# Optimization experiments

Measured on AMD Instinct MI355X. Metric: run time of the kernel, lower is better.

The kernel has to match this reference:

```python
import jax, jax.numpy as jnp
import numpy as np
import math

HIDDEN = 2048
NUM_HEADS = 16
NUM_KV_HEADS = 4
HEAD_DIM = 128
GROUPS = NUM_HEADS // NUM_KV_HEADS
BATCH = 1
SEQ = 4096
THETA = 10000.0


def _rope(x):
    # x: [B, h, S, D], interleaved-pair rotation as in the torch module
    seq = x.shape[2]
    freqs = 1.0 / (THETA ** (jnp.arange(0, HEAD_DIM, 2, dtype=jnp.float32) / HEAD_DIM))  # [D/2]
    angles = jnp.arange(seq, dtype=jnp.float32)[:, None] * freqs[None, :]  # [S, D/2]
    cos = jnp.cos(angles)[None, None]  # [1,1,S,D/2]
    sin = jnp.sin(angles)[None, None]
    x1 = x[..., 0::2]
    x2 = x[..., 1::2]
    # stack along new last axis then flatten -> interleaved layout
    rot = jnp.stack([x1 * cos - x2 * sin, x1 * sin + x2 * cos], axis=-1)
    return rot.reshape(x.shape)


def setup_inputs() -> dict:
    key = jax.random.key(0)
    kx, kq, kk, kv, ko = jax.random.split(key, 5)
    scale = 0.02
    x = jax.random.normal(kx, (BATCH, SEQ, HIDDEN), dtype=jnp.float32)
    Wq = jax.random.normal(kq, (NUM_HEADS * HEAD_DIM, HIDDEN), dtype=jnp.float32) * scale
    Wk = jax.random.normal(kk, (NUM_KV_HEADS * HEAD_DIM, HIDDEN), dtype=jnp.float32) * scale
    Wv = jax.random.normal(kv, (NUM_KV_HEADS * HEAD_DIM, HIDDEN), dtype=jnp.float32) * scale
    Wo = jax.random.normal(ko, (HIDDEN, NUM_HEADS * HEAD_DIM), dtype=jnp.float32) * scale
    return {"x": x, "Wq": Wq, "Wk": Wk, "Wv": Wv, "Wo": Wo}


def reference(x, Wq, Wk, Wv, Wo):
    B, S, _ = x.shape
    q = (x @ Wq.T).reshape(B, S, NUM_HEADS, HEAD_DIM).transpose(0, 2, 1, 3)      # [B,16,S,D]
    k = (x @ Wk.T).reshape(B, S, NUM_KV_HEADS, HEAD_DIM).transpose(0, 2, 1, 3)   # [B,4,S,D]
    v = (x @ Wv.T).reshape(B, S, NUM_KV_HEADS, HEAD_DIM).transpose(0, 2, 1, 3)
    q = _rope(q)
    k = _rope(k)
    # GQA: repeat_interleave KV heads across the group dim
    k = jnp.repeat(k, GROUPS, axis=1)  # [B,16,S,D]
    v = jnp.repeat(v, GROUPS, axis=1)
    scale = 1.0 / math.sqrt(HEAD_DIM)
    scores = jnp.einsum("bhqd,bhkd->bhqk", q, k) * scale  # [B,16,S,S]
    causal = jnp.triu(jnp.ones((S, S), dtype=bool), k=1)
    scores = jnp.where(causal[None, None], jnp.float32(-jnp.inf), scores)
    attn = jax.nn.softmax(scores, axis=-1)
    out = jnp.einsum("bhqk,bhkd->bhqd", attn, v)           # [B,16,S,D]
    out = out.transpose(0, 2, 1, 3).reshape(B, S, NUM_HEADS * HEAD_DIM)
    return out @ Wo.T
```

## Files before the change

### kernel.cpp

```cpp
#include <hip/hip_runtime.h>
#include <hip/hip_bf16.h>

typedef unsigned short u16;
typedef unsigned int u32;
typedef short short8 __attribute__((ext_vector_type(8)));
typedef unsigned short ushort4v __attribute__((ext_vector_type(4)));
typedef float f32x4 __attribute__((ext_vector_type(4)));
typedef float f32x16 __attribute__((ext_vector_type(16)));
typedef u32 u32x4 __attribute__((ext_vector_type(4)));

#define SEQN 4096
#define HID 2048
#define NH 16
#define NKV 4
#define HD 128
#define QDIM 2048
#define KVD 512
#define QKVS 3072

static __device__ __forceinline__ float bf2f(u16 u){
  unsigned x = ((unsigned)u) << 16; float f; __builtin_memcpy(&f, &x, 4); return f;
}
static __device__ __forceinline__ u16 f2bf(float f){
  unsigned x; __builtin_memcpy(&x, &f, 4);
  x += 0x7fffu + ((x >> 16) & 1u);
  return (u16)(x >> 16);
}
static __device__ __forceinline__ u32 pk2(float a, float b){
  return (u32)f2bf(a) | ((u32)f2bf(b) << 16);
}

__global__ __launch_bounds__(256) void cvt_kernel(const float* __restrict__ in, u16* __restrict__ out, int n4){
  int i = blockIdx.x * 256 + threadIdx.x;
  if (i >= n4) return;
  f32x4 v = ((const f32x4*)in)[i];
  ushort4v o;
  o.x = f2bf(v.x); o.y = f2bf(v.y); o.z = f2bf(v.z); o.w = f2bf(v.w);
  ((ushort4v*)out)[i] = o;
}

__global__ __launch_bounds__(256) void rope_kernel(u16* __restrict__ X, int stride, int nheads, int total){
  int idx = blockIdx.x * 256 + threadIdx.x;
  if (idx >= total) return;
  int i = idx & 63;
  int rest = idx >> 6;
  int h = rest % nheads;
  int s = rest / nheads;
  float freq = expf(-0.14391156831212788f * (float)i);
  float ang = (float)s * freq;
  float c = cosf(ang), sn = sinf(ang);
  u16* p = X + (size_t)s * stride + (size_t)h * HD + 2 * i;
  float x1 = bf2f(p[0]), x2 = bf2f(p[1]);
  p[0] = f2bf(x1 * c - x2 * sn);
  p[1] = f2bf(x1 * sn + x2 * c);
}

__global__ __launch_bounds__(256) void vtrans_kernel(const u16* __restrict__ V, int vstride, u16* __restrict__ VTg){
  __shared__ u16 T[64][72];
  const int s0 = blockIdx.x * 64;
  const int c0 = blockIdx.y * 64;
  const int tid = threadIdx.x;
  const int sl = tid & 63, ch = tid >> 6;
  const u16* src = V + (size_t)(s0 + sl) * vstride + c0 + ch * 16;
  *(short8*)&T[sl][ch * 16]     = *(const short8*)(src);
  *(short8*)&T[sl][ch * 16 + 8] = *(const short8*)(src + 8);
  __syncthreads();
#pragma unroll
  for (int it = 0; it < 16; it++){
    int c = it * 4 + ch;
    VTg[(size_t)(c0 + c) * SEQN + s0 + sl] = T[sl][c];
  }
}

static __device__ __forceinline__ void gload16(const void* g, void* l){
  __builtin_amdgcn_global_load_lds((const __attribute__((address_space(1))) void*)g,
                                   (__attribute__((address_space(3))) void*)l, 16, 0, 0);
}

template<int F32OUT>
__global__ __launch_bounds__(256) void gemm_kernel(const u16* __restrict__ A, const u16* __restrict__ B,
                                                   void* __restrict__ Cout, int M, int N, int Kd, int ldc){
  __shared__ alignas(16) u16 As[128 * 32];
  __shared__ alignas(16) u16 Bs[128 * 32];
  const int tid = threadIdx.x;
  const int w = tid >> 6, l = tid & 63;
  const int wr = w >> 1, wc = w & 1;
  const int lc = l & 15, lg = l >> 4;
  const int tm = blockIdx.x * 128, tn = blockIdx.y * 128;

  const int srow = w * 32 + (l >> 2);
  const int scol = (l & 3) * 8;
  const u16* Ag = A + (size_t)(tm + srow) * Kd + scol;
  const u16* Bg = B + (size_t)(tn + srow) * Kd + scol;
  u16* As0 = As + (w * 2) * 512;
  u16* Bs0 = Bs + (w * 2) * 512;

  f32x4 acc[4][4] = {};

  for (int k0 = 0; k0 < Kd; k0 += 32){
    gload16(Ag + k0,                    As0);
    gload16(Ag + k0 + (size_t)16 * Kd,  As0 + 512);
    gload16(Bg + k0,                    Bs0);
    gload16(Bg + k0 + (size_t)16 * Kd,  Bs0 + 512);
    __syncthreads();
    short8 a[4], b[4];
#pragma unroll
    for (int mi = 0; mi < 4; mi++) a[mi] = *(const short8*)&As[(wr*64 + mi*16 + lc) * 32 + lg*8];
#pragma unroll
    for (int ni = 0; ni < 4; ni++) b[ni] = *(const short8*)&Bs[(wc*64 + ni*16 + lc) * 32 + lg*8];
#pragma unroll
    for (int mi = 0; mi < 4; mi++)
#pragma unroll
      for (int ni = 0; ni < 4; ni++)
        acc[mi][ni] = __builtin_amdgcn_mfma_f32_16x16x32_bf16(a[mi], b[ni], acc[mi][ni], 0, 0, 0);
    __syncthreads();
  }

#pragma unroll
  for (int mi = 0; mi < 4; mi++)
#pragma unroll
    for (int ni = 0; ni < 4; ni++)
#pragma unroll
      for (int r = 0; r < 4; r++){
        int row = tm + wr*64 + mi*16 + lg*4 + r;
        int col = tn + wc*64 + ni*16 + lc;
        float v = acc[mi][ni][r];
        if (F32OUT) ((float*)Cout)[(size_t)row * ldc + col] = v;
        else        ((u16*)Cout)[(size_t)row * ldc + col] = f2bf(v);
      }
}

__global__ __launch_bounds__(256, 2) void attn_kernel(const u16* __restrict__ Qg, const u16* __restrict__ Kgb,
                                                      const u16* __restrict__ VTg, u16* __restrict__ Aout,
                                                      u16* __restrict__ PO, float* __restrict__ mP,
                                                      float* __restrict__ LP){
  __shared__ alignas(16) char pool[65536];

  const int pr  = blockIdx.x;
  const int h   = blockIdx.y;
  const int s   = blockIdx.z;
  const int kvh = h >> 2;
  const int tid = threadIdx.x;
  const int w = tid >> 6, l = tid & 63;
  const int q5 = l & 31;
  const int hi = l >> 5;
  const int hi4 = hi * 4;
  const float csc = 0.12751743f;

  const u16* Ksrc[4];
  const u16* Vsrc[4];
#pragma unroll
  for (int i = 0; i < 4; i++){
    int blk = w * 4 + i;
    int row = blk * 4 + (l >> 4);
    int cg  = (l & 15) ^ (row & 15);
    Ksrc[i] = Kgb + (size_t)row * QKVS + kvh * HD + cg * 8;
    int d   = blk * 8 + (l >> 3);
    int cv  = (l & 7) ^ (d & 7);
    Vsrc[i] = VTg + (size_t)(kvh * 128 + d) * SEQN + cv * 8;
  }

  auto issueTile = [&](int b, int kv0){
    char* Ksb = pool + b * 32768;
    char* VTb = Ksb + 16384;
#pragma unroll
    for (int i = 0; i < 4; i++)
      gload16(Ksrc[i] + (size_t)kv0 * QKVS, Ksb + (w * 4 + i) * 1024);
#pragma unroll
    for (int i = 0; i < 4; i++)
      gload16(Vsrc[i] + kv0, VTb + (w * 4 + i) * 1024);
  };

  const int qlo = pr, qhi = 31 - pr;
  int nseg, sq[2], st0[2], st1[2], smode[2];
  if (s == 0){
    nseg = 2;
    sq[0] = qlo; st0[0] = 0;           st1[0] = 2 * pr + 2;   smode[0] = 0;
    sq[1] = qhi; st0[1] = 0;           st1[1] = 31 - 2 * pr;  smode[1] = 1;
  } else {
    nseg = 1;
    sq[0] = qhi; st0[0] = 31 - 2 * pr; st1[0] = 64 - 2 * pr;  smode[0] = 2;
  }

  for (int sg = 0; sg < nseg; sg++){
    const int qt = sq[sg], t0 = st0[sg], t1 = st1[sg], mode = smode[sg];
    const int qbase = qt * 128 + w * 32;
    const int qa    = qbase + q5;

    short8 qf[8];
    {
      const u16* qp = Qg + (size_t)(qbase + q5) * QKVS + h * HD + hi * 8;
#pragma unroll
      for (int k0 = 0; k0 < 8; k0++) qf[k0] = *(const short8*)(qp + k0 * 16);
    }

    f32x16 Ov[4] = {};
    float Lrow = 0.f;
    float ms = -1e30f;

    auto computeTile = [&](int b, int kv0){
      if (kv0 > qbase + 31) return;
      char* Ksb = pool + b * 32768;
      char* VTb = Ksb + 16384;
      f32x16 Sv[2] = {};
#pragma unroll
      for (int k0 = 0; k0 < 8; k0++){
#pragma unroll
        for (int nb = 0; nb < 2; nb++){
          int kvr = nb * 32 + q5;
          short8 kf = *(const short8*)(Ksb + kvr * 256 + (((k0 * 2 + hi) ^ (kvr & 15)) << 4));
          Sv[nb] = __builtin_amdgcn_mfma_f32_32x32x16_bf16(kf, qf[k0], Sv[nb], 0, 0, 0);
        }
      }
      if (kv0 + 63 > qbase){
#pragma unroll
        for (int nb = 0; nb < 2; nb++)
#pragma unroll
          for (int r = 0; r < 16; r++){
            int kva = kv0 + nb * 32 + (r & 3) + 8 * (r >> 2) + hi4;
            if (kva > qa) Sv[nb][r] = -1e30f;
          }
      }
      float tm = -3e38f;
#pragma unroll
      for (int nb = 0; nb < 2; nb++)
#pragma unroll
        for (int r = 0; r < 16; r++) tm = fmaxf(tm, Sv[nb][r]);
      tm = fmaxf(tm, __shfl_xor(tm, 32));
      float tms = tm * csc;
      if (!__all(tms - ms <= 8.f)){
        float nms = fmaxf(ms, tms);
        float al = __builtin_amdgcn_exp2f(ms - nms);
        ms = nms;
        Lrow *= al;
#pragma unroll
        for (int nb = 0; nb < 4; nb++)
#pragma unroll
          for (int r = 0; r < 16; r++) Ov[nb][r] *= al;
      }
      float ts = 0.f;
#pragma unroll
      for (int nb = 0; nb < 2; nb++)
#pragma unroll
        for (int r = 0; r < 16; r++){
          float p = __builtin_amdgcn_exp2f(__builtin_fmaf(Sv[nb][r], csc, -ms));
          Sv[nb][r] = p;
          ts += p;
        }
      ts += __shfl_xor(ts, 32);
      Lrow += ts;
#pragma unroll
      for (int kc = 0; kc < 4; kc++){
        const int nb = kc >> 1, rb = (kc & 1) * 8;
        u32 Aw = pk2(Sv[nb][rb + 0], Sv[nb][rb + 1]);
        u32 Bw = pk2(Sv[nb][rb + 2], Sv[nb][rb + 3]);
        u32 Cw = pk2(Sv[nb][rb + 4], Sv[nb][rb + 5]);
        u32 Dw = pk2(Sv[nb][rb + 6], Sv[nb][rb + 7]);
        u32 sAw = __shfl_xor(Aw, 32);
        u32 sBw = __shfl_xor(Bw, 32);
        u32 sCw = __shfl_xor(Cw, 32);
        u32 sDw = __shfl_xor(Dw, 32);
        u32 w0 = hi ? sCw : Aw;
        u32 w1 = hi ? sDw : Bw;
        u32 w2 = hi ? Cw : sAw;
        u32 w3 = hi ? Dw : sBw;
        u32x4 pw4 = {w0, w1, w2, w3};
        short8 pf = *(short8*)&pw4;
#pragma unroll
        for (int nbd = 0; nbd < 4; nbd++){
          int drow = nbd * 32 + q5;
          short8 vf = *(const short8*)(VTb + drow * 128 + (((kc * 2 + hi) ^ (drow & 7)) << 4));
          Ov[nbd] = __builtin_amdgcn_mfma_f32_32x32x16_bf16(vf, pf, Ov[nbd], 0, 0, 0);
        }
      }
    };

    __syncthreads();
    issueTile(0, t0 * 64);
    __syncthreads();
    int cur = 0;
    for (int t = t0; t < t1; t++){
      if (t + 1 < t1) issueTile(cur ^ 1, (t + 1) * 64);
      computeTile(cur, t * 64);
      __syncthreads();
      cur ^= 1;
    }

    u16* Ew = (u16*)(pool + w * 8704);
    float rl = (mode == 0) ? (1.f / Lrow) : 1.f;
#pragma unroll
    for (int nbd = 0; nbd < 4; nbd++)
#pragma unroll
      for (int r = 0; r < 16; r += 2){
        int d = nbd * 32 + (r & 3) + 8 * (r >> 2) + hi4;
        u32 wpk = pk2(Ov[nbd][r] * rl, Ov[nbd][r + 1] * rl);
        *(u32*)((char*)Ew + q5 * 272 + d * 2) = wpk;
      }
    if (mode == 0){
#pragma unroll
      for (int pass = 0; pass < 8; pass++){
        int q2 = pass * 4 + (l >> 4);
        short8 ov = *(const short8*)((char*)Ew + q2 * 272 + (l & 15) * 16);
        *(short8*)(Aout + (size_t)(qbase + q2) * QDIM + h * HD + (l & 15) * 8) = ov;
      }
    } else {
      const int p = mode - 1;
      u16* dstb = PO + ((size_t)((p * 16 + pr) * NH + h) * 128) * 128;
#pragma unroll
      for (int pass = 0; pass < 8; pass++){
        int q2 = pass * 4 + (l >> 4);
        short8 ov = *(const short8*)((char*)Ew + q2 * 272 + (l & 15) * 16);
        *(short8*)(dstb + (size_t)(w * 32 + q2) * 128 + (l & 15) * 8) = ov;
      }
      if (hi == 0){
        int idx = ((p * 16 + pr) * NH + h) * 128 + w * 32 + q5;
        mP[idx] = ms;
        LP[idx] = Lrow;
      }
    }
  }
}

__global__ __launch_bounds__(256) void combine_kernel(const u16* __restrict__ PO, const float* __restrict__ mP,
                                                      const float* __restrict__ LP, u16* __restrict__ Aout){
  const int pr = blockIdx.x;
  const int h  = blockIdx.y;
  const int tid = threadIdx.x;
  const int r  = tid >> 1;
  const int dh = (tid & 1) * 64;
  const int qhi = 31 - pr;
  const int idx0 = ((0 * 16 + pr) * NH + h) * 128 + r;
  const int idx1 = ((1 * 16 + pr) * NH + h) * 128 + r;
  float m0 = mP[idx0], m1 = mP[idx1];
  float L0 = LP[idx0], L1 = LP[idx1];
  float M = fmaxf(m0, m1);
  float a0 = __builtin_amdgcn_exp2f(m0 - M);
  float a1 = __builtin_amdgcn_exp2f(m1 - M);
  float rl = 1.f / (L0 * a0 + L1 * a1);
  const u16* o0 = PO + (size_t)idx0 * 128 + dh;
  const u16* o1 = PO + (size_t)idx1 * 128 + dh;
  u16* dst = Aout + (size_t)(qhi * 128 + r) * QDIM + h * HD + dh;
#pragma unroll
  for (int ch = 0; ch < 8; ch++){
    short8 v0 = *(const short8*)(o0 + ch * 8);
    short8 v1 = *(const short8*)(o1 + ch * 8);
    short8 ov;
#pragma unroll
    for (int j = 0; j < 8; j++)
      ov[j] = (short)f2bf((bf2f((u16)v0[j]) * a0 + bf2f((u16)v1[j]) * a1) * rl);
    *(short8*)(dst + ch * 8) = ov;
  }
}

extern "C" void kernel_launch(void* const* d_in, const int* in_sizes, int n_in,
                              void* d_out, int out_size, void* d_ws, size_t ws_size,
                              hipStream_t stream){
  const float* x  = (const float*)d_in[0];
  const float* Wq = (const float*)d_in[1];
  const float* Wk = (const float*)d_in[2];
  const float* Wv = (const float*)d_in[3];
  const float* Wo = (const float*)d_in[4];

  char* p = (char*)d_ws;
  u16* xb    = (u16*)p; p += (size_t)SEQN * HID * 2;
  u16* Wqkvb = (u16*)p; p += (size_t)QKVS * HID * 2;
  u16* Wob   = (u16*)p; p += (size_t)HID * QDIM * 2;
  u16* QKVb  = (u16*)p; p += (size_t)SEQN * QKVS * 2;
  u16* Ab    = (u16*)p; p += (size_t)SEQN * QDIM * 2;
  u16* VTg   = (u16*)p; p += (size_t)SEQN * KVD * 2;
  u16* PO    = (u16*)p; p += (size_t)2 * 16 * NH * 128 * 128 * 2;
  float* mP  = (float*)p; p += (size_t)2 * 16 * NH * 128 * 4;
  float* LP  = (float*)p; p += (size_t)2 * 16 * NH * 128 * 4;

  cvt_kernel<<<(SEQN*HID/4 + 255)/256, 256, 0, stream>>>(x,  xb,  SEQN*HID/4);
  cvt_kernel<<<(QDIM*HID/4 + 255)/256, 256, 0, stream>>>(Wq, Wqkvb,                         QDIM*HID/4);
  cvt_kernel<<<(KVD*HID/4 + 255)/256, 256, 0, stream>>>(Wk, Wqkvb + (size_t)QDIM*HID,       KVD*HID/4);
  cvt_kernel<<<(KVD*HID/4 + 255)/256, 256, 0, stream>>>(Wv, Wqkvb + (size_t)(QDIM+KVD)*HID, KVD*HID/4);
  cvt_kernel<<<(HID*QDIM/4 + 255)/256, 256, 0, stream>>>(Wo, Wob, HID*QDIM/4);

  gemm_kernel<0><<<dim3(SEQN/128, QKVS/128), 256, 0, stream>>>(xb, Wqkvb, QKVb, SEQN, QKVS, HID, QKVS);

  rope_kernel<<<(SEQN*NH*64)/256,  256, 0, stream>>>(QKVb,        QKVS, NH,  SEQN*NH*64);
  rope_kernel<<<(SEQN*NKV*64)/256, 256, 0, stream>>>(QKVb + QDIM, QKVS, NKV, SEQN*NKV*64);

  vtrans_kernel<<<dim3(SEQN/64, KVD/64), 256, 0, stream>>>(QKVb + QDIM + KVD, QKVS, VTg);

  attn_kernel<<<dim3(16, NH, 2), 256, 0, stream>>>(QKVb, QKVb + QDIM, VTg, Ab, PO, mP, LP);
  combine_kernel<<<dim3(16, NH), 256, 0, stream>>>(PO, mP, LP, Ab);

  gemm_kernel<1><<<dim3(SEQN/128, HID/128), 256, 0, stream>>>(Ab, Wob, d_out, SEQN, HID, QDIM, HID);
}
```

Baseline: 267.0 us.

## Merge conversion and rope launches, vectorize rope, stage bf16 GEMM epilogue through LDS

Replaces the five float-to-bf16 conversion launches with one kernel that dispatches on global index, and the two rope launches with one kernel that handles Q and K heads with 16-byte vector loads and stores, eight elements per thread. The bf16-output GEMM epilogue now writes accumulators into padded shared memory per wave and then emits 16-byte coalesced row stores instead of scattered 2-byte stores. This is meant to cut launch overhead and the cost of narrow uncoalesced memory traffic. It adds an extra barrier and shared-memory round trip in the GEMM epilogue.

```diff
diff --git a/kernel.cpp b/kernel.cpp
--- a/kernel.cpp
+++ b/kernel.cpp
@@ -30,29 +30,51 @@
   return (u32)f2bf(a) | ((u32)f2bf(b) << 16);
 }
 
-__global__ __launch_bounds__(256) void cvt_kernel(const float* __restrict__ in, u16* __restrict__ out, int n4){
-  int i = blockIdx.x * 256 + threadIdx.x;
-  if (i >= n4) return;
-  f32x4 v = ((const f32x4*)in)[i];
+#define G1 (SEQN*HID/4)
+#define G2 (QDIM*HID/4)
+#define G3 (KVD*HID/4)
+#define G4 (KVD*HID/4)
+#define G5 (HID*QDIM/4)
+__global__ __launch_bounds__(256) void cvt5_kernel(const float* __restrict__ x,  const float* __restrict__ Wq,
+                                                   const float* __restrict__ Wk, const float* __restrict__ Wv,
+                                                   const float* __restrict__ Wo, u16* __restrict__ xb,
+                                                   u16* __restrict__ Wqkvb, u16* __restrict__ Wob){
+  int g = blockIdx.x * 256 + threadIdx.x;
+  const float* src; u16* dst; int off;
+  if (g < G1)                { src = x;  dst = xb;    off = g; }
+  else if (g < G1+G2)        { src = Wq; dst = Wqkvb; off = g - G1; }
+  else if (g < G1+G2+G3)     { src = Wk; dst = Wqkvb + (size_t)QDIM*HID;        off = g - (G1+G2); }
+  else if (g < G1+G2+G3+G4)  { src = Wv; dst = Wqkvb + (size_t)(QDIM+KVD)*HID;  off = g - (G1+G2+G3); }
+  else if (g < G1+G2+G3+G4+G5){ src = Wo; dst = Wob;  off = g - (G1+G2+G3+G4); }
+  else return;
+  f32x4 v = ((const f32x4*)src)[off];
   ushort4v o;
   o.x = f2bf(v.x); o.y = f2bf(v.y); o.z = f2bf(v.z); o.w = f2bf(v.w);
-  ((ushort4v*)out)[i] = o;
-}
-
-__global__ __launch_bounds__(256) void rope_kernel(u16* __restrict__ X, int stride, int nheads, int total){
+  ((ushort4v*)dst)[off] = o;
+}
+
+__global__ __launch_bounds__(256) void rope2_kernel(u16* __restrict__ QKVb){
   int idx = blockIdx.x * 256 + threadIdx.x;
-  if (idx >= total) return;
-  int i = idx & 63;
-  int rest = idx >> 6;
-  int h = rest % nheads;
-  int s = rest / nheads;
-  float freq = expf(-0.14391156831212788f * (float)i);
-  float ang = (float)s * freq;
-  float c = cosf(ang), sn = sinf(ang);
-  u16* p = X + (size_t)s * stride + (size_t)h * HD + 2 * i;
-  float x1 = bf2f(p[0]), x2 = bf2f(p[1]);
-  p[0] = f2bf(x1 * c - x2 * sn);
-  p[1] = f2bf(x1 * sn + x2 * c);
+  if (idx >= SEQN * (NH + NKV) * 16) return;
+  int i8 = idx & 15;
+  int rest = idx >> 4;
+  int h = rest % (NH + NKV);
+  int s = rest / (NH + NKV);
+  int col = (h < NH) ? h * HD : QDIM + (h - NH) * HD;
+  u16* p = QKVb + (size_t)s * QKVS + col + i8 * 8;
+  short8 v = *(const short8*)p;
+  short8 o;
+#pragma unroll
+  for (int j = 0; j < 4; j++){
+    int i = i8 * 4 + j;
+    float freq = expf(-0.14391156831212788f * (float)i);
+    float ang = (float)s * freq;
+    float c = cosf(ang), sn = sinf(ang);
+    float x1 = bf2f((u16)v[2*j]), x2 = bf2f((u16)v[2*j+1]);
+    o[2*j]   = (short)f2bf(x1 * c - x2 * sn);
+    o[2*j+1] = (short)f2bf(x1 * sn + x2 * c);
+  }
+  *(short8*)p = o;
 }
 
 __global__ __launch_bounds__(256) void vtrans_kernel(const u16* __restrict__ V, int vstride, u16* __restrict__ VTg){
@@ -80,8 +102,9 @@
 template<int F32OUT>
 __global__ __launch_bounds__(256) void gemm_kernel(const u16* __restrict__ A, const u16* __restrict__ B,
                                                    void* __restrict__ Cout, int M, int N, int Kd, int ldc){
-  __shared__ alignas(16) u16 As[128 * 32];
-  __shared__ alignas(16) u16 Bs[128 * 32];
+  __shared__ alignas(16) u16 sh[8192];
+  u16* As = sh;
+  u16* Bs = sh + 4096;
   const int tid = threadIdx.x;
   const int w = tid >> 6, l = tid & 63;
   const int wr = w >> 1, wc = w & 1;
@@ -116,18 +139,37 @@
     __syncthreads();
   }
 
-#pragma unroll
-  for (int mi = 0; mi < 4; mi++)
-#pragma unroll
-    for (int ni = 0; ni < 4; ni++)
-#pragma unroll
-      for (int r = 0; r < 4; r++){
-        int row = tm + wr*64 + mi*16 + lg*4 + r;
-        int col = tn + wc*64 + ni*16 + lc;
-        float v = acc[mi][ni][r];
-        if (F32OUT) ((float*)Cout)[(size_t)row * ldc + col] = v;
-        else        ((u16*)Cout)[(size_t)row * ldc + col] = f2bf(v);
-      }
+  if (F32OUT){
+#pragma unroll
+    for (int mi = 0; mi < 4; mi++)
+#pragma unroll
+      for (int ni = 0; ni < 4; ni++)
+#pragma unroll
+        for (int r = 0; r < 4; r++){
+          int row = tm + wr*64 + mi*16 + lg*4 + r;
+          int col = tn + wc*64 + ni*16 + lc;
+          ((float*)Cout)[(size_t)row * ldc + col] = acc[mi][ni][r];
+        }
+  } else {
+    __syncthreads();
+    u16* Ew = sh + w * 1168;
+#pragma unroll
+    for (int mi = 0; mi < 4; mi++){
+#pragma unroll
+      for (int ni = 0; ni < 4; ni++)
+#pragma unroll
+        for (int r = 0; r < 4; r++)
+          Ew[(lg * 4 + r) * 73 + ni * 16 + lc] = f2bf(acc[mi][ni][r]);
+#pragma unroll
+      for (int pass = 0; pass < 2; pass++){
+        int row = pass * 8 + (l >> 3);
+        short8 v;
+#pragma unroll
+        for (int j = 0; j < 8; j++) v[j] = (short)Ew[row * 73 + (l & 7) * 8 + j];
+        *(short8*)((u16*)Cout + (size_t)(tm + wr*64 + mi*16 + row) * ldc + tn + wc*64 + (l & 7) * 8) = v;
+      }
+    }
+  }
 }
 
 __global__ __launch_bounds__(256, 2) void attn_kernel(const u16* __restrict__ Qg, const u16* __restrict__ Kgb,
@@ -372,16 +414,12 @@
   float* mP  = (float*)p; p += (size_t)2 * 16 * NH * 128 * 4;
   float* LP  = (float*)p; p += (size_t)2 * 16 * NH * 128 * 4;
 
-  cvt_kernel<<<(SEQN*HID/4 + 255)/256, 256, 0, stream>>>(x,  xb,  SEQN*HID/4);
-  cvt_kernel<<<(QDIM*HID/4 + 255)/256, 256, 0, stream>>>(Wq, Wqkvb,                         QDIM*HID/4);
-  cvt_kernel<<<(KVD*HID/4 + 255)/256, 256, 0, stream>>>(Wk, Wqkvb + (size_t)QDIM*HID,       KVD*HID/4);
-  cvt_kernel<<<(KVD*HID/4 + 255)/256, 256, 0, stream>>>(Wv, Wqkvb + (size_t)(QDIM+KVD)*HID, KVD*HID/4);
-  cvt_kernel<<<(HID*QDIM/4 + 255)/256, 256, 0, stream>>>(Wo, Wob, HID*QDIM/4);
+  const int totg = G1 + G2 + G3 + G4 + G5;
+  cvt5_kernel<<<(totg + 255) / 256, 256, 0, stream>>>(x, Wq, Wk, Wv, Wo, xb, Wqkvb, Wob);
 
   gemm_kernel<0><<<dim3(SEQN/128, QKVS/128), 256, 0, stream>>>(xb, Wqkvb, QKVb, SEQN, QKVS, HID, QKVS);
 
-  rope_kernel<<<(SEQN*NH*64)/256,  256, 0, stream>>>(QKVb,        QKVS, NH,  SEQN*NH*64);
-  rope_kernel<<<(SEQN*NKV*64)/256, 256, 0, stream>>>(QKVb + QDIM, QKVS, NKV, SEQN*NKV*64);
+  rope2_kernel<<<(SEQN*(NH+NKV)*16 + 255) / 256, 256, 0, stream>>>(QKVb);
 
   vtrans_kernel<<<dim3(SEQN/64, KVD/64), 256, 0, stream>>>(QKVb + QDIM + KVD, QKVS, VTg);
 
```

Measured after the change: 257.5 us. 3.5% less time.
